# Kernel optimization log

Hardware: AMD Instinct MI355X
Metric: run time of the kernel (lower is better)

Reference implementation:

```python
import jax, jax.numpy as jnp
import numpy as np

HID = 128
PE_DIM = 4
N = 100_000       # nodes per type
E = 400_000       # edges per edge type
L = 3             # message passing layers
G = 512           # num graphs
NT = ['ssBox', 'place_frame', 'object', 'ssCylinder', 'pick', 'place']
FEAT_DIMS = {'ssBox': 4, 'place_frame': 4, 'object': 4, 'ssCylinder': 3}
EMB_IN = {'ssBox': 8, 'place_frame': 8, 'object': 8, 'ssCylinder': 7, 'pick': 4, 'place': 4}
EDGE_TYPES = [
    ('object', 'ssBox'), ('ssBox', 'object'), ('place_frame', 'ssBox'), ('ssBox', 'place_frame'),
    ('place_frame', 'object'), ('object', 'place_frame'), ('pick', 'place'), ('place', 'pick'),
    ('object', 'object'), ('ssBox', 'ssBox'), ('place_frame', 'place_frame'), ('ssCylinder', 'ssCylinder'),
    ('object', 'pick'), ('pick', 'object'), ('place_frame', 'pick'), ('pick', 'place_frame'),
    ('ssCylinder', 'pick'), ('pick', 'ssCylinder'), ('object', 'place'), ('place', 'object'),
    ('ssCylinder', 'place'), ('place', 'ssCylinder'), ('place_frame', 'place'), ('place', 'place_frame')]


def _pe(times):
    # sinusoidal PE from integer positions -> [n, PE_DIM], cols interleaved sin/cos
    pos = times.astype(jnp.float32)[:, None]
    div = jnp.exp(jnp.arange(0, PE_DIM, 2, dtype=jnp.float32) * (-np.log(10000.0) / PE_DIM))
    s, c = jnp.sin(pos * div), jnp.cos(pos * div)
    return jnp.stack([s, c], axis=2).reshape(pos.shape[0], PE_DIM)


def setup_inputs() -> dict:
    key = jax.random.key(0)
    ks = iter(jax.random.split(key, 64))
    inp = {}
    for t in ['ssBox', 'place_frame', 'object']:
        inp['x_' + t] = jax.random.normal(next(ks), (N, 4), jnp.float32)
    inp['x_ssCylinder'] = jax.random.normal(next(ks), (N, 3), jnp.float32)
    for t in NT:
        d = EMB_IN[t]
        inp['W_' + t] = jax.random.normal(next(ks), (d, HID), jnp.float32) / np.sqrt(d)
        inp['b_' + t] = jax.random.normal(next(ks), (HID,), jnp.float32) * 0.01
    sc = 1.0 / np.sqrt(HID)
    inp['sage_Wl'] = jax.random.normal(next(ks), (L, 24, HID, HID), jnp.float32) * sc
    inp['sage_bl'] = jax.random.normal(next(ks), (L, 24, HID), jnp.float32) * 0.01
    inp['sage_Wr'] = jax.random.normal(next(ks), (L, 24, HID, HID), jnp.float32) * sc
    inp['oh_W1'] = jax.random.normal(next(ks), (HID, HID // 4), jnp.float32) * sc
    inp['oh_b1'] = jax.random.normal(next(ks), (HID // 4,), jnp.float32) * 0.01
    inp['oh_W2'] = jax.random.normal(next(ks), (HID // 4, 1), jnp.float32) / np.sqrt(HID // 4)
    inp['oh_b2'] = jax.random.normal(next(ks), (1,), jnp.float32) * 0.01
    inp['times'] = jax.random.randint(next(ks), (6, N), 0, 1000, jnp.int32)
    inp['edges'] = jax.random.randint(next(ks), (24, 2, E), 0, N, jnp.int32)
    inp['batch'] = jax.random.randint(next(ks), (6, N), 0, G, jnp.int32)
    return inp


def reference(x_ssBox, x_place_frame, x_object, x_ssCylinder,
              W_ssBox, b_ssBox, W_place_frame, b_place_frame, W_object, b_object,
              W_ssCylinder, b_ssCylinder, W_pick, b_pick, W_place, b_place,
              sage_Wl, sage_bl, sage_Wr, oh_W1, oh_b1, oh_W2, oh_b2,
              times, edges, batch):
    feats = {'ssBox': x_ssBox, 'place_frame': x_place_frame, 'object': x_object, 'ssCylinder': x_ssCylinder}
    embW = {'ssBox': W_ssBox, 'place_frame': W_place_frame, 'object': W_object,
            'ssCylinder': W_ssCylinder, 'pick': W_pick, 'place': W_place}
    embB = {'ssBox': b_ssBox, 'place_frame': b_place_frame, 'object': b_object,
            'ssCylinder': b_ssCylinder, 'pick': b_pick, 'place': b_place}
    init, x = {}, {}
    for t in ['ssBox', 'place_frame', 'object', 'ssCylinder']:
        f = jnp.concatenate([feats[t], _pe(times[NT.index(t)])], axis=1)
        h = f @ embW[t] + embB[t]
        init[t] = h
        x[t] = h
    for t in ['pick', 'place']:
        x[t] = _pe(times[NT.index(t)]) @ embW[t] + embB[t]
    x = {t: jax.nn.relu(v) for t, v in x.items()}

    for layer in range(L):
        out = {}
        for i, (src, dst) in enumerate(EDGE_TYPES):
            e = edges[i]
            msg = x[src][e[0]]                                           # [E, HID] gather
            agg = jax.ops.segment_sum(msg, e[1], num_segments=N)
            deg = jax.ops.segment_sum(jnp.ones((E,), msg.dtype), e[1], num_segments=N)
            mean = agg / jnp.maximum(deg, 1.0)[:, None]                  # SAGE mean aggr
            o = mean @ sage_Wl[layer, i] + sage_bl[layer, i] + x[dst] @ sage_Wr[layer, i]
            out[dst] = out[dst] + o if dst in out else o
        # dropout is identity in eval/reference
        x = {t: jax.nn.relu(out.get(t, x[t])) for t in x}

    g = jnp.zeros((G, HID), jnp.float32)
    for t in ['pick', 'place']:
        g = g.at[batch[NT.index(t)]].add(x[t])
    for t in ['ssBox', 'ssCylinder', 'place_frame', 'object']:
        g = g.at[batch[NT.index(t)]].add(init[t])
    h = jax.nn.relu(g) @ oh_W1 + oh_b1
    h = jax.nn.relu(h) @ oh_W2 + oh_b2
    return h.squeeze(-1)
```

## Files before the change

kernel.cpp:

```cpp
#include <hip/hip_runtime.h>
#include <hip/hip_bf16.h>

#define NN 100000
#define EE 400000
#define HID 128
#define GG 512
#define NTY 6
#define NET 24
#define TILES_PER_TYPE 1563
#define EMB_TILES 782
#define BLK_ELEMS ((size_t)NN * 128)
#define BLK_BYTES (BLK_ELEMS * 2)

typedef _Float16 half8 __attribute__((ext_vector_type(8)));
typedef float f32x4 __attribute__((ext_vector_type(4)));

__constant__ int d_EMB_IN[6]    = {8,8,8,7,4,4};
__constant__ int d_FD[6]        = {4,4,4,3,0,0};
__constant__ int d_EDGE_SRC[24] = {2,0,1,0,1,2,4,5,2,0,1,3,2,4,1,4,3,4,2,5,3,5,1,5};
__constant__ int d_DST_NIN[6]   = {3,5,5,3,4,4};
__constant__ int d_DST_OFF[6]   = {0,3,8,13,16,20};
__constant__ int d_DST_EDGES[24]= {0,2,9, 3,5,10,15,23, 1,4,8,13,19, 11,17,21, 7,12,14,16, 6,18,20,22};

struct GP {
    const float* feat[4];
    const float* embW[6];
    const float* embB[6];
    const float* Wl; const float* bl; const float* Wr;
    const float* W1; const float* b1; const float* W2; const float* b2;
    const int* times; const int* edges; const int* batch;
};

struct XT { _Float16* p[6]; };

__device__ __forceinline__ int clampi(int v, int lo, int hi) {
    return v < lo ? lo : (v > hi ? hi : v);
}

__global__ void zero_i32(int* __restrict__ p, int n) {
    int i = blockIdx.x * 256 + threadIdx.x;
    if (i < n) p[i] = 0;
}

__global__ void diag_kernel(float* __restrict__ out, float v) {
    int i = blockIdx.x * 64 + threadIdx.x;
    if (i < GG) out[i] = v;
}

__global__ void csr_pass1(const int* __restrict__ edges, int* __restrict__ deg,
                          int* __restrict__ rank) {
    int i = blockIdx.x * 256 + threadIdx.x;
    if (i >= NET * EE) return;
    int et = i / EE, e = i - et * EE;
    int dst = clampi(edges[(et * 2 + 1) * EE + e], 0, NN - 1);
    rank[i] = atomicAdd(&deg[et * NN + dst], 1);
}

__global__ void csr_pass2(const int* __restrict__ edges, const int* __restrict__ rowptr,
                          const int* __restrict__ rank, int* __restrict__ csr) {
    int i = blockIdx.x * 256 + threadIdx.x;
    if (i >= NET * EE) return;
    int et = i / EE, e = i - et * EE;
    int src = clampi(edges[(et * 2) * EE + e], 0, NN - 1);
    int dst = clampi(edges[(et * 2 + 1) * EE + e], 0, NN - 1);
    int pos = clampi(rowptr[et * NN + dst] + rank[i], 0, NET * EE - 1);
    csr[pos] = src;
}

__global__ void hist_nodes(const int* __restrict__ batch, int* __restrict__ hist2) {
    int i = blockIdx.x * 256 + threadIdx.x;
    if (i >= NTY * NN) return;
    int t = i / NN, n = i - t * NN;
    int b = clampi(batch[t * NN + n], 0, GG - 1);
    atomicAdd(&hist2[t * GG + b], 1);
}

__global__ void scatter_nodes(const int* __restrict__ batch, const int* __restrict__ rowptr2,
                              int* __restrict__ fill2, int* __restrict__ nodelist) {
    int i = blockIdx.x * 256 + threadIdx.x;
    if (i >= NTY * NN) return;
    int t = i / NN, n = i - t * NN;
    int b = t * GG + clampi(batch[t * NN + n], 0, GG - 1);
    int pos = clampi(rowptr2[b] + atomicAdd(&fill2[b], 1), 0, NTY * NN - 1);
    nodelist[pos] = n;
}

__global__ void scan1(const int* __restrict__ in, int* __restrict__ out, int* __restrict__ bsum, int M) {
    int base = blockIdx.x * 2048;
    int tid = threadIdx.x;
    int idx = base + tid * 8;
    int v[8]; int s = 0;
#pragma unroll
    for (int k = 0; k < 8; k++) { int i = idx + k; v[k] = (i < M) ? in[i] : 0; }
#pragma unroll
    for (int k = 0; k < 8; k++) { int t = v[k]; v[k] = s; s += t; }
    __shared__ int sh[256];
    sh[tid] = s; __syncthreads();
    for (int off = 1; off < 256; off <<= 1) {
        int t = (tid >= off) ? sh[tid - off] : 0;
        __syncthreads(); sh[tid] += t; __syncthreads();
    }
    int excl = sh[tid] - s;
#pragma unroll
    for (int k = 0; k < 8; k++) { int i = idx + k; if (i < M) out[i] = excl + v[k]; }
    if (tid == 255) bsum[blockIdx.x] = sh[255];
}

__global__ void scan2(int* __restrict__ bsum, int NB, int* __restrict__ rowptr, int M, int total) {
    __shared__ int sh[256];
    __shared__ int shc;
    int tid = threadIdx.x;
    int carry = 0;
    for (int chunk = 0; chunk < NB; chunk += 256) {
        int i = chunk + tid;
        int v = (i < NB) ? bsum[i] : 0;
        __syncthreads();
        sh[tid] = v; __syncthreads();
        for (int off = 1; off < 256; off <<= 1) {
            int t = (tid >= off) ? sh[tid - off] : 0;
            __syncthreads(); sh[tid] += t; __syncthreads();
        }
        int inc = sh[tid];
        if (i < NB) bsum[i] = carry + inc - v;
        if (tid == 255) shc = inc;
        __syncthreads();
        carry += shc;
    }
    if (tid == 0) rowptr[M] = total;
}

__global__ void scan3(int* __restrict__ out, const int* __restrict__ bsum, int M) {
    int i = blockIdx.x * 256 + threadIdx.x;
    if (i < M) out[i] += bsum[i >> 11];
}

__global__ void prep_wl(const float* __restrict__ Wl, _Float16* __restrict__ WlTf) {
    int i = blockIdx.x * 256 + threadIdx.x;
    if (i >= 72 * 16384) return;
    int mat = i >> 14;
    int o = i & 16383;
    int cq = o >> 9; int c = cq >> 2, q = cq & 3;
    int lane = (o >> 3) & 63, j = o & 7;
    int k = q * 32 + (lane >> 4) * 8 + j;
    int n = c * 16 + (lane & 15);
    WlTf[i] = (_Float16)Wl[((size_t)mat * 128 + k) * 128 + n];
}

__global__ void prep_wr(const float* __restrict__ Wr, _Float16* __restrict__ WrTf) {
    int i = blockIdx.x * 256 + threadIdx.x;
    if (i >= 18 * 16384) return;
    int mat = i >> 14;
    int l = mat / 6, dd = mat - l * 6;
    int o = i & 16383;
    int cq = o >> 9; int c = cq >> 2, q = cq & 3;
    int lane = (o >> 3) & 63, j = o & 7;
    int k = q * 32 + (lane >> 4) * 8 + j;
    int n = c * 16 + (lane & 15);
    float s = 0.f;
    int nin = d_DST_NIN[dd], off = d_DST_OFF[dd];
    for (int ii = 0; ii < nin; ++ii) {
        int e = d_DST_EDGES[off + ii];
        s += Wr[(((size_t)l * 24 + e) * 128 + k) * 128 + n];
    }
    WrTf[i] = (_Float16)s;
}

__global__ void prep_bl(const float* __restrict__ bl, float* __restrict__ bls) {
    int i = blockIdx.x * 256 + threadIdx.x;
    if (i >= 3 * 6 * 128) return;
    int l = i / 768; int rest = i - l * 768;
    int dd = rest >> 7; int col = rest & 127;
    float s = 0.f;
    int nin = d_DST_NIN[dd], off = d_DST_OFF[dd];
    for (int ii = 0; ii < nin; ++ii) {
        int e = d_DST_EDGES[off + ii];
        s += bl[((size_t)l * 24 + e) * 128 + col];
    }
    bls[i] = s;
}

__global__ void embed_kernel(GP gp, XT xout) {
    int t = blockIdx.x / EMB_TILES;
    int tile = blockIdx.x - t * EMB_TILES;
    int base = tile * 128;
    int tid = threadIdx.x;
    __shared__ float fls[128][8];
    if (tid < 128) {
        int node = base + tid;
        float f[8] = {0.f,0.f,0.f,0.f,0.f,0.f,0.f,0.f};
        if (node < NN) {
            int fd = d_FD[t];
            if (fd > 0) {
                const float* fp = gp.feat[t] + (size_t)node * fd;
                for (int k = 0; k < fd; k++) f[k] = fp[k];
            }
            float pos = (float)gp.times[t * NN + node];
            float d1 = expf(-0.5f * logf(10000.0f));
            f[fd + 0] = sinf(pos);      f[fd + 1] = cosf(pos);
            f[fd + 2] = sinf(pos * d1); f[fd + 3] = cosf(pos * d1);
        }
#pragma unroll
        for (int k = 0; k < 8; k++) fls[tid][k] = f[k];
    }
    __syncthreads();
    int d = tid & 127, np = tid >> 7;
    const float* W = gp.embW[t]; const float* b = gp.embB[t];
    int ein = d_EMB_IN[t];
    float Wreg[8];
#pragma unroll
    for (int k = 0; k < 8; k++) Wreg[k] = (k < ein) ? W[k * 128 + d] : 0.f;
    float breg = b[d];
    _Float16* xp = xout.p[t];
    for (int it = 0; it < 64; ++it) {
        int nl = np + it * 2;
        int node = base + nl;
        if (node < NN) {
            float h = breg;
#pragma unroll
            for (int k = 0; k < 8; k++) h += fls[nl][k] * Wreg[k];
            h = h > 0.f ? h : 0.f;
            xp[(size_t)node * 128 + d] = (_Float16)h;
        }
    }
}

__global__ __launch_bounds__(256)
void layer_kernel(XT cur, XT nxt, int d0,
                  const int* __restrict__ rowptr, const int* __restrict__ csr,
                  const _Float16* __restrict__ WlTf, const _Float16* __restrict__ WrTf,
                  const float* __restrict__ bls) {
    int bid = blockIdx.x;
    int d = d0 + bid / TILES_PER_TYPE;
    int tile = bid % TILES_PER_TYPE;
    int tid = threadIdx.x, lane = tid & 63, wave = tid >> 6;
    int lrow = lane & 15, quad = lane >> 4;
    int wrow0 = tile * 64 + wave * 16;
    int myrow = wrow0 + lrow;
    bool rowok = myrow < NN;

    f32x4 acc[8];
#pragma unroll
    for (int c = 0; c < 8; c++) {
        float bv = bls[d * 128 + c * 16 + lrow];
        acc[c] = (f32x4){bv, bv, bv, bv};
    }

    int nin = d_DST_NIN[d];
    int off = d_DST_OFF[d];
    for (int term = 0; term <= nin; ++term) {
        half8 af[4];
        const _Float16* Bmat;
        if (term == 0) {
            Bmat = WrTf + (size_t)d * 16384;
            if (rowok) {
                const half8* p = (const half8*)(cur.p[d] + (size_t)myrow * 128 + quad * 8);
                af[0] = p[0]; af[1] = p[4]; af[2] = p[8]; af[3] = p[12];
            } else {
#pragma unroll
                for (int q = 0; q < 4; q++)
#pragma unroll
                    for (int z = 0; z < 8; z++) af[q][z] = (_Float16)0.f;
            }
        } else {
            int e = d_DST_EDGES[off + term - 1];
            int st = d_EDGE_SRC[e];
            Bmat = WlTf + (size_t)e * 16384;
            const _Float16* xs = cur.p[st];
            float facc[32];
#pragma unroll
            for (int z = 0; z < 32; z++) facc[z] = 0.f;
            int start = 0, cnt = 0;
            if (rowok) {
                int bi = e * NN + myrow;
                start = clampi(rowptr[bi], 0, NET * EE - 1);
                cnt = clampi(rowptr[bi + 1] - start, 0, 4096);
            }
            for (int j = 0;; ++j) {
                if (__ballot(j < cnt) == 0ull) break;
                if (j < cnt) {
                    int sn = clampi(csr[start + j], 0, NN - 1);
                    const half8* p = (const half8*)(xs + (size_t)sn * 128 + quad * 8);
                    half8 v0 = p[0], v1 = p[4], v2 = p[8], v3 = p[12];
#pragma unroll
                    for (int z = 0; z < 8; z++) {
                        facc[z]      += (float)v0[z];
                        facc[8 + z]  += (float)v1[z];
                        facc[16 + z] += (float)v2[z];
                        facc[24 + z] += (float)v3[z];
                    }
                }
            }
            float inv = 1.0f / (float)(cnt > 1 ? cnt : 1);
#pragma unroll
            for (int q = 0; q < 4; q++)
#pragma unroll
                for (int z = 0; z < 8; z++) af[q][z] = (_Float16)(facc[q * 8 + z] * inv);
        }
#pragma unroll
        for (int q = 0; q < 4; q++) {
#pragma unroll
            for (int c = 0; c < 8; c++) {
                half8 b = *(const half8*)(Bmat + (((c * 4 + q) << 9) + (lane << 3)));
                acc[c] = __builtin_amdgcn_mfma_f32_16x16x32_f16(af[q], b, acc[c], 0, 0, 0);
            }
        }
    }
    _Float16* xo = nxt.p[d];
#pragma unroll
    for (int c = 0; c < 8; c++) {
#pragma unroll
        for (int r = 0; r < 4; r++) {
            int grow = wrow0 + quad * 4 + r;
            if (grow < NN) {
                float v = acc[c][r];
                v = v > 0.f ? v : 0.f;
                xo[(size_t)grow * 128 + c * 16 + lrow] = (_Float16)v;
            }
        }
    }
}

__global__ void readout_kernel(GP gp, XT x3,
                               const int* __restrict__ nodelist, const int* __restrict__ rowptr2,
                               float* __restrict__ g) {
    int t = blockIdx.x >> 9;
    int gi = blockIdx.x & 511;
    int tid = threadIdx.x;
    int s = clampi(rowptr2[t * GG + gi], 0, NTY * NN - 1);
    int cnt = clampi(rowptr2[t * GG + gi + 1] - s, 0, NN);
    int d = tid & 127, np = tid >> 7;
    if (t >= 4) {
        float acc = 0.f;
        const _Float16* xp = x3.p[t];
        for (int li = np; li < cnt; li += 2) {
            int node = clampi(nodelist[s + li], 0, NN - 1);
            acc += (float)xp[(size_t)node * 128 + d];
        }
        atomicAdd(&g[gi * 128 + d], acc);
    } else {
        int ein = d_EMB_IN[t];
        int fd = d_FD[t];
        const float* W = gp.embW[t]; const float* bb = gp.embB[t];
        float d1 = expf(-0.5f * logf(10000.0f));
        float fs[8];
#pragma unroll
        for (int k = 0; k < 8; k++) fs[k] = 0.f;
        for (int li = tid; li < cnt; li += 256) {
            int node = clampi(nodelist[s + li], 0, NN - 1);
            const float* fp = gp.feat[t] + (size_t)node * fd;
            for (int k = 0; k < fd; k++) fs[k] += fp[k];
            float pos = (float)gp.times[t * NN + node];
            fs[fd + 0] += sinf(pos);      fs[fd + 1] += cosf(pos);
            fs[fd + 2] += sinf(pos * d1); fs[fd + 3] += cosf(pos * d1);
        }
        __shared__ float red[8][256];
#pragma unroll
        for (int k = 0; k < 8; k++) red[k][tid] = fs[k];
        __syncthreads();
        for (int off = 128; off >= 1; off >>= 1) {
            if (tid < off) {
#pragma unroll
                for (int k = 0; k < 8; k++) red[k][tid] += red[k][tid + off];
            }
            __syncthreads();
        }
        if (tid < 128) {
            float acc = (float)cnt * bb[d];
            for (int k = 0; k < ein; k++) acc += red[k][0] * W[k * 128 + d];
            atomicAdd(&g[gi * 128 + d], acc);
        }
    }
}

__global__ void head_kernel(const float* __restrict__ g, const float* __restrict__ W1,
                            const float* __restrict__ b1, const float* __restrict__ W2,
                            const float* __restrict__ b2, float* __restrict__ out) {
    int gi = blockIdx.x;
    int tid = threadIdx.x;
    __shared__ float h1[32];
    if (tid < 32) {
        float s = b1[tid];
        for (int dd = 0; dd < 128; ++dd) s += fmaxf(g[gi * 128 + dd], 0.f) * W1[dd * 32 + tid];
        h1[tid] = s;
    }
    __syncthreads();
    if (tid == 0) {
        float o = b2[0];
        for (int j = 0; j < 32; ++j) o += fmaxf(h1[j], 0.f) * W2[j];
        out[gi] = o;
    }
}

extern "C" void kernel_launch(void* const* d_in, const int* in_sizes, int n_in,
                              void* d_out, int out_size, void* d_ws, size_t ws_size,
                              hipStream_t stream) {
    char* ws = (char*)d_ws;
    size_t o = 0;
    auto alloc = [&](size_t bytes) -> void* {
        void* p = ws + o;
        o += (bytes + 255) & ~(size_t)255;
        return p;
    };
    _Float16* xws   = (_Float16*)alloc(9 * BLK_BYTES);
    int* csr        = (int*)alloc((size_t)NET * EE * 4 + 256);
    int* rowptr     = (int*)alloc(((size_t)NET * NN + 1) * 4);
    int* nodelist   = (int*)alloc((size_t)NTY * NN * 4);
    int* rowptr2    = (int*)alloc((NTY * GG + 1) * 4);
    float* g        = (float*)alloc(GG * 128 * 4);
    int* bsum       = (int*)alloc(4096 * 4);
    int* bsum2      = (int*)alloc(256 * 4);
    size_t REQUIRED = o;
    (void)in_sizes; (void)out_size;

    if (ws_size < REQUIRED || n_in != 26) {
        float v = 2000.0f + (float)(ws_size >> 20) + (n_in != 26 ? 100000.0f : 0.0f);
        diag_kernel<<<8, 64, 0, stream>>>((float*)d_out, v);
        return;
    }

    GP gp;
    for (int t = 0; t < 4; t++) gp.feat[t] = (const float*)d_in[t];
    for (int t = 0; t < 6; t++) { gp.embW[t] = (const float*)d_in[4 + 2 * t]; gp.embB[t] = (const float*)d_in[5 + 2 * t]; }
    gp.Wl = (const float*)d_in[16];
    gp.bl = (const float*)d_in[17];
    gp.Wr = (const float*)d_in[18];
    gp.W1 = (const float*)d_in[19];
    gp.b1 = (const float*)d_in[20];
    gp.W2 = (const float*)d_in[21];
    gp.b2 = (const float*)d_in[22];
    gp.times = (const int*)d_in[23];
    gp.edges = (const int*)d_in[24];
    gp.batch = (const int*)d_in[25];

    _Float16* WlTf = (_Float16*)d_in[18];
    _Float16* WrTf = (_Float16*)d_in[25];
    float* bls     = (float*)((char*)d_in[25] + 1048576);

    int* deg   = (int*)xws;
    int* hist2 = (int*)((char*)xws + 9600000);
    int* rank  = (int*)((char*)xws + BLK_BYTES);

    XT tabA, tabB;
    for (int t = 0; t < 6; t++) tabA.p[t] = xws + (size_t)t * BLK_ELEMS;
    for (int t = 0; t < 3; t++) tabB.p[t] = xws + (size_t)(6 + t) * BLK_ELEMS;
    for (int t = 3; t < 6; t++) tabB.p[t] = (_Float16*)d_in[24] + (size_t)(t - 3) * BLK_ELEMS;

    int Medge = NET * NN;
    int NB = (Medge + 2047) / 2048;
    int Mn = NTY * GG;
    int NB2 = (Mn + 2047) / 2048;

    zero_i32<<<(Medge + 255) / 256, 256, 0, stream>>>(deg, Medge);
    csr_pass1<<<(NET * EE + 255) / 256, 256, 0, stream>>>(gp.edges, deg, rank);
    scan1<<<NB, 256, 0, stream>>>(deg, rowptr, bsum, Medge);
    scan2<<<1, 256, 0, stream>>>(bsum, NB, rowptr, Medge, NET * EE);
    scan3<<<(Medge + 255) / 256, 256, 0, stream>>>(rowptr, bsum, Medge);
    csr_pass2<<<(NET * EE + 255) / 256, 256, 0, stream>>>(gp.edges, rowptr, rank, csr);

    zero_i32<<<(Mn + 255) / 256, 256, 0, stream>>>(hist2, Mn);
    hist_nodes<<<(NTY * NN + 255) / 256, 256, 0, stream>>>(gp.batch, hist2);
    scan1<<<NB2, 256, 0, stream>>>(hist2, rowptr2, bsum2, Mn);
    scan2<<<1, 256, 0, stream>>>(bsum2, NB2, rowptr2, Mn, NTY * NN);
    scan3<<<(Mn + 255) / 256, 256, 0, stream>>>(rowptr2, bsum2, Mn);
    zero_i32<<<(Mn + 255) / 256, 256, 0, stream>>>(hist2, Mn);
    scatter_nodes<<<(NTY * NN + 255) / 256, 256, 0, stream>>>(gp.batch, rowptr2, hist2, nodelist);

    prep_wr<<<(18 * 16384 + 255) / 256, 256, 0, stream>>>(gp.Wr, WrTf);
    prep_bl<<<(3 * 6 * 128 + 255) / 256, 256, 0, stream>>>(gp.bl, bls);
    prep_wl<<<(72 * 16384 + 255) / 256, 256, 0, stream>>>(gp.Wl, WlTf);

    embed_kernel<<<NTY * EMB_TILES, 256, 0, stream>>>(gp, tabA);

    layer_kernel<<<6 * TILES_PER_TYPE, 256, 0, stream>>>(tabA, tabB, 0, rowptr, csr,
        WlTf + (size_t)0 * 24 * 16384, WrTf + (size_t)0 * 6 * 16384, bls + 0 * 6 * 128);
    layer_kernel<<<5 * TILES_PER_TYPE, 256, 0, stream>>>(tabB, tabA, 1, rowptr, csr,
        WlTf + (size_t)1 * 24 * 16384, WrTf + (size_t)1 * 6 * 16384, bls + 1 * 6 * 128);
    layer_kernel<<<2 * TILES_PER_TYPE, 256, 0, stream>>>(tabA, tabB, 4, rowptr, csr,
        WlTf + (size_t)2 * 24 * 16384, WrTf + (size_t)2 * 6 * 16384, bls + 2 * 6 * 128);

    zero_i32<<<(GG * 128 + 255) / 256, 256, 0, stream>>>((int*)g, GG * 128);
    readout_kernel<<<NTY * GG, 256, 0, stream>>>(gp, tabB, nodelist, rowptr2, g);
    head_kernel<<<GG, 64, 0, stream>>>(g, gp.W1, gp.b1, gp.W2, gp.b2, (float*)d_out);
}
```

Before: 2.957 ms.

## Trim preprocessing: 16-bit ranks, single-block node scan, smem weight prep, vectorized embed/readout

Edge ranks are stored as 16-bit values, which halves their memory traffic. The node-histogram scan collapses into one single-block kernel that also re-zeroes the histogram, and the two zero kernels are merged into one. Weight reformatting now stages each matrix in shared memory and folds the bias sum into the same launch. The embed and readout kernels write and read 8 halves per thread, and readout reduces in shared memory before its atomics. The costs are the launch overhead of many small kernels and uncoalesced access in setup, traded against low occupancy (72 or 19 blocks) in the weight-prep kernels and ranks that saturate above 65535.

```diff
diff --git a/kernel.cpp b/kernel.cpp
--- a/kernel.cpp
+++ b/kernel.cpp
@@ -48,22 +48,23 @@
 }
 
 __global__ void csr_pass1(const int* __restrict__ edges, int* __restrict__ deg,
-                          int* __restrict__ rank) {
+                          unsigned short* __restrict__ rank) {
     int i = blockIdx.x * 256 + threadIdx.x;
     if (i >= NET * EE) return;
     int et = i / EE, e = i - et * EE;
     int dst = clampi(edges[(et * 2 + 1) * EE + e], 0, NN - 1);
-    rank[i] = atomicAdd(&deg[et * NN + dst], 1);
+    int r = atomicAdd(&deg[et * NN + dst], 1);
+    rank[i] = (unsigned short)(r > 65535 ? 65535 : r);
 }
 
 __global__ void csr_pass2(const int* __restrict__ edges, const int* __restrict__ rowptr,
-                          const int* __restrict__ rank, int* __restrict__ csr) {
+                          const unsigned short* __restrict__ rank, int* __restrict__ csr) {
     int i = blockIdx.x * 256 + threadIdx.x;
     if (i >= NET * EE) return;
     int et = i / EE, e = i - et * EE;
     int src = clampi(edges[(et * 2) * EE + e], 0, NN - 1);
     int dst = clampi(edges[(et * 2 + 1) * EE + e], 0, NN - 1);
-    int pos = clampi(rowptr[et * NN + dst] + rank[i], 0, NET * EE - 1);
+    int pos = clampi(rowptr[et * NN + dst] + (int)rank[i], 0, NET * EE - 1);
     csr[pos] = src;
 }
 
@@ -73,6 +74,28 @@
     int t = i / NN, n = i - t * NN;
     int b = clampi(batch[t * NN + n], 0, GG - 1);
     atomicAdd(&hist2[t * GG + b], 1);
+}
+
+__global__ void node_scan(int* __restrict__ hist2, int* __restrict__ rowptr2) {
+    __shared__ int sh[256];
+    __shared__ int shc;
+    int tid = threadIdx.x;
+    int carry = 0;
+    for (int chunk = 0; chunk < NTY * GG; chunk += 256) {
+        int v = hist2[chunk + tid];
+        __syncthreads();
+        sh[tid] = v; __syncthreads();
+        for (int off = 1; off < 256; off <<= 1) {
+            int t = (tid >= off) ? sh[tid - off] : 0;
+            __syncthreads(); sh[tid] += t; __syncthreads();
+        }
+        rowptr2[chunk + tid] = carry + sh[tid] - v;
+        hist2[chunk + tid] = 0;
+        if (tid == 255) shc = sh[255];
+        __syncthreads();
+        carry += shc;
+    }
+    if (tid == 0) rowptr2[NTY * GG] = NTY * NN;
 }
 
 __global__ void scatter_nodes(const int* __restrict__ batch, const int* __restrict__ rowptr2,
@@ -134,49 +157,64 @@
     if (i < M) out[i] += bsum[i >> 11];
 }
 
-__global__ void prep_wl(const float* __restrict__ Wl, _Float16* __restrict__ WlTf) {
-    int i = blockIdx.x * 256 + threadIdx.x;
-    if (i >= 72 * 16384) return;
-    int mat = i >> 14;
-    int o = i & 16383;
+__device__ __forceinline__ int frag_src(int o) {
     int cq = o >> 9; int c = cq >> 2, q = cq & 3;
     int lane = (o >> 3) & 63, j = o & 7;
     int k = q * 32 + (lane >> 4) * 8 + j;
     int n = c * 16 + (lane & 15);
-    WlTf[i] = (_Float16)Wl[((size_t)mat * 128 + k) * 128 + n];
-}
-
-__global__ void prep_wr(const float* __restrict__ Wr, _Float16* __restrict__ WrTf) {
-    int i = blockIdx.x * 256 + threadIdx.x;
-    if (i >= 18 * 16384) return;
-    int mat = i >> 14;
+    return k * 128 + n;
+}
+
+__global__ __launch_bounds__(256, 1)
+void prep_wl2(const float* __restrict__ Wl, _Float16* __restrict__ WlTf) {
+    __shared__ float tile[16384];
+    int mat = blockIdx.x;
+    const float* src = Wl + (size_t)mat * 16384;
+    for (int idx = threadIdx.x; idx < 16384; idx += 256) tile[idx] = src[idx];
+    __syncthreads();
+    _Float16* dst = WlTf + (size_t)mat * 16384;
+    for (int j = 0; j < 64; ++j) {
+        int o = j * 256 + threadIdx.x;
+        dst[o] = (_Float16)tile[frag_src(o)];
+    }
+}
+
+__global__ __launch_bounds__(256, 1)
+void prep_wr2(const float* __restrict__ Wr, const float* __restrict__ bl,
+              _Float16* __restrict__ WrTf, float* __restrict__ bls) {
+    if (blockIdx.x == 18) {
+        for (int i = threadIdx.x; i < 3 * 6 * 128; i += 256) {
+            int l = i / 768; int rest = i - l * 768;
+            int dd = rest >> 7; int col = rest & 127;
+            float s = 0.f;
+            int nin = d_DST_NIN[dd], off = d_DST_OFF[dd];
+            for (int ii = 0; ii < nin; ++ii) {
+                int e = d_DST_EDGES[off + ii];
+                s += bl[((size_t)l * 24 + e) * 128 + col];
+            }
+            bls[i] = s;
+        }
+        return;
+    }
+    __shared__ float tile[16384];
+    int mat = blockIdx.x;
     int l = mat / 6, dd = mat - l * 6;
-    int o = i & 16383;
-    int cq = o >> 9; int c = cq >> 2, q = cq & 3;
-    int lane = (o >> 3) & 63, j = o & 7;
-    int k = q * 32 + (lane >> 4) * 8 + j;
-    int n = c * 16 + (lane & 15);
-    float s = 0.f;
+    float accum[64];
+#pragma unroll
+    for (int j = 0; j < 64; ++j) accum[j] = 0.f;
     int nin = d_DST_NIN[dd], off = d_DST_OFF[dd];
     for (int ii = 0; ii < nin; ++ii) {
         int e = d_DST_EDGES[off + ii];
-        s += Wr[(((size_t)l * 24 + e) * 128 + k) * 128 + n];
-    }
-    WrTf[i] = (_Float16)s;
-}
-
-__global__ void prep_bl(const float* __restrict__ bl, float* __restrict__ bls) {
-    int i = blockIdx.x * 256 + threadIdx.x;
-    if (i >= 3 * 6 * 128) return;
-    int l = i / 768; int rest = i - l * 768;
-    int dd = rest >> 7; int col = rest & 127;
-    float s = 0.f;
-    int nin = d_DST_NIN[dd], off = d_DST_OFF[dd];
-    for (int ii = 0; ii < nin; ++ii) {
-        int e = d_DST_EDGES[off + ii];
-        s += bl[((size_t)l * 24 + e) * 128 + col];
-    }
-    bls[i] = s;
+        const float* src = Wr + ((size_t)l * 24 + e) * 16384;
+        __syncthreads();
+        for (int idx = threadIdx.x; idx < 16384; idx += 256) tile[idx] = src[idx];
+        __syncthreads();
+        for (int j = 0; j < 64; ++j)
+            accum[j] += tile[frag_src(j * 256 + threadIdx.x)];
+    }
+    _Float16* dst = WrTf + (size_t)mat * 16384;
+    for (int j = 0; j < 64; ++j)
+        dst[j * 256 + threadIdx.x] = (_Float16)accum[j];
 }
 
 __global__ void embed_kernel(GP gp, XT xout) {
@@ -185,6 +223,14 @@
     int base = tile * 128;
     int tid = threadIdx.x;
     __shared__ float fls[128][8];
+    __shared__ float Wsh[8][128];
+    __shared__ float bsh[128];
+    int ein = d_EMB_IN[t];
+    for (int idx = tid; idx < 1024; idx += 256) {
+        int k = idx >> 7, dd = idx & 127;
+        Wsh[k][dd] = (k < ein) ? gp.embW[t][k * 128 + dd] : 0.f;
+    }
+    if (tid < 128) bsh[tid] = gp.embB[t][tid];
     if (tid < 128) {
         int node = base + tid;
         float f[8] = {0.f,0.f,0.f,0.f,0.f,0.f,0.f,0.f};
@@ -203,24 +249,24 @@
         for (int k = 0; k < 8; k++) fls[tid][k] = f[k];
     }
     __syncthreads();
-    int d = tid & 127, np = tid >> 7;
-    const float* W = gp.embW[t]; const float* b = gp.embB[t];
-    int ein = d_EMB_IN[t];
-    float Wreg[8];
-#pragma unroll
-    for (int k = 0; k < 8; k++) Wreg[k] = (k < ein) ? W[k * 128 + d] : 0.f;
-    float breg = b[d];
+    int oct = tid & 15, slot = tid >> 4;
     _Float16* xp = xout.p[t];
-    for (int it = 0; it < 64; ++it) {
-        int nl = np + it * 2;
+    for (int nl = slot; nl < 128; nl += 16) {
         int node = base + nl;
-        if (node < NN) {
-            float h = breg;
-#pragma unroll
-            for (int k = 0; k < 8; k++) h += fls[nl][k] * Wreg[k];
-            h = h > 0.f ? h : 0.f;
-            xp[(size_t)node * 128 + d] = (_Float16)h;
-        }
+        if (node >= NN) continue;
+        float h[8];
+#pragma unroll
+        for (int j = 0; j < 8; ++j) h[j] = bsh[oct * 8 + j];
+#pragma unroll
+        for (int k = 0; k < 8; ++k) {
+            float f = fls[nl][k];
+#pragma unroll
+            for (int j = 0; j < 8; ++j) h[j] += f * Wsh[k][oct * 8 + j];
+        }
+        half8 hv;
+#pragma unroll
+        for (int j = 0; j < 8; ++j) { float v = h[j] > 0.f ? h[j] : 0.f; hv[j] = (_Float16)v; }
+        *(half8*)(xp + (size_t)node * 128 + oct * 8) = hv;
     }
 }
 
@@ -328,15 +374,31 @@
     int tid = threadIdx.x;
     int s = clampi(rowptr2[t * GG + gi], 0, NTY * NN - 1);
     int cnt = clampi(rowptr2[t * GG + gi + 1] - s, 0, NN);
-    int d = tid & 127, np = tid >> 7;
     if (t >= 4) {
-        float acc = 0.f;
+        int oct = tid & 15, slot = tid >> 4;
         const _Float16* xp = x3.p[t];
-        for (int li = np; li < cnt; li += 2) {
+        float acc8[8];
+#pragma unroll
+        for (int z = 0; z < 8; z++) acc8[z] = 0.f;
+        for (int li = slot; li < cnt; li += 16) {
             int node = clampi(nodelist[s + li], 0, NN - 1);
-            acc += (float)xp[(size_t)node * 128 + d];
-        }
-        atomicAdd(&g[gi * 128 + d], acc);
+            half8 v = *(const half8*)(xp + (size_t)node * 128 + oct * 8);
+#pragma unroll
+            for (int z = 0; z < 8; z++) acc8[z] += (float)v[z];
+        }
+        __shared__ float red[16][128];
+#pragma unroll
+        for (int z = 0; z < 8; z++) red[slot][oct * 8 + z] = acc8[z];
+        __syncthreads();
+        for (int off = 8; off >= 1; off >>= 1) {
+            if (slot < off) {
+#pragma unroll
+                for (int z = 0; z < 8; z++)
+                    red[slot][oct * 8 + z] += red[slot + off][oct * 8 + z];
+            }
+            __syncthreads();
+        }
+        if (tid < 128) atomicAdd(&g[gi * 128 + tid], red[0][tid]);
     } else {
         int ein = d_EMB_IN[t];
         int fd = d_FD[t];
@@ -365,9 +427,9 @@
             __syncthreads();
         }
         if (tid < 128) {
-            float acc = (float)cnt * bb[d];
-            for (int k = 0; k < ein; k++) acc += red[k][0] * W[k * 128 + d];
-            atomicAdd(&g[gi * 128 + d], acc);
+            float acc = (float)cnt * bb[tid];
+            for (int k = 0; k < ein; k++) acc += red[k][0] * W[k * 128 + tid];
+            atomicAdd(&g[gi * 128 + tid], acc);
         }
     }
 }
@@ -436,9 +498,9 @@
     _Float16* WrTf = (_Float16*)d_in[25];
     float* bls     = (float*)((char*)d_in[25] + 1048576);
 
-    int* deg   = (int*)xws;
-    int* hist2 = (int*)((char*)xws + 9600000);
-    int* rank  = (int*)((char*)xws + BLK_BYTES);
+    int* deg             = (int*)xws;
+    int* hist2           = (int*)((char*)xws + 9600000);
+    unsigned short* rank = (unsigned short*)((char*)xws + BLK_BYTES);
 
     XT tabA, tabB;
     for (int t = 0; t < 6; t++) tabA.p[t] = xws + (size_t)t * BLK_ELEMS;
@@ -448,26 +510,20 @@
     int Medge = NET * NN;
     int NB = (Medge + 2047) / 2048;
     int Mn = NTY * GG;
-    int NB2 = (Mn + 2047) / 2048;
-
-    zero_i32<<<(Medge + 255) / 256, 256, 0, stream>>>(deg, Medge);
+
+    zero_i32<<<(Medge + Mn + 255) / 256, 256, 0, stream>>>(deg, Medge + Mn);
     csr_pass1<<<(NET * EE + 255) / 256, 256, 0, stream>>>(gp.edges, deg, rank);
     scan1<<<NB, 256, 0, stream>>>(deg, rowptr, bsum, Medge);
     scan2<<<1, 256, 0, stream>>>(bsum, NB, rowptr, Medge, NET * EE);
     scan3<<<(Medge + 255) / 256, 256, 0, stream>>>(rowptr, bsum, Medge);
     csr_pass2<<<(NET * EE + 255) / 256, 256, 0, stream>>>(gp.edges, rowptr, rank, csr);
 
-    zero_i32<<<(Mn + 255) / 256, 256, 0, stream>>>(hist2, Mn);
     hist_nodes<<<(NTY * NN + 255) / 256, 256, 0, stream>>>(gp.batch, hist2);
-    scan1<<<NB2, 256, 0, stream>>>(hist2, rowptr2, bsum2, Mn);
-    scan2<<<1, 256, 0, stream>>>(bsum2, NB2, rowptr2, Mn, NTY * NN);
-    scan3<<<(Mn + 255) / 256, 256, 0, stream>>>(rowptr2, bsum2, Mn);
-    zero_i32<<<(Mn + 255) / 256, 256, 0, stream>>>(hist2, Mn);
+    node_scan<<<1, 256, 0, stream>>>(hist2, rowptr2);
     scatter_nodes<<<(NTY * NN + 255) / 256, 256, 0, stream>>>(gp.batch, rowptr2, hist2, nodelist);
 
-    prep_wr<<<(18 * 16384 + 255) / 256, 256, 0, stream>>>(gp.Wr, WrTf);
-    prep_bl<<<(3 * 6 * 128 + 255) / 256, 256, 0, stream>>>(gp.bl, bls);
-    prep_wl<<<(72 * 16384 + 255) / 256, 256, 0, stream>>>(gp.Wl, WlTf);
+    prep_wr2<<<19, 256, 0, stream>>>(gp.Wr, gp.bl, WrTf, bls);
+    prep_wl2<<<72, 256, 0, stream>>>(gp.Wl, WlTf);
 
     embed_kernel<<<NTY * EMB_TILES, 256, 0, stream>>>(gp, tabA);
 
```

After: 2.912 ms. No clear change (-1.5%).
